# Kernel optimization log

Hardware: AMD Instinct MI355X
Metric: run time of the kernel (lower is better)

The kernel has to match this reference:

```python
import jax, jax.numpy as jnp
import numpy as np

N_NODES = 50000
N_EDGES = 800000
F_DIM = 128
H_DIM = 128


def setup_inputs() -> dict:
    key = jax.random.key(0)
    ks = jax.random.split(key, 14)
    sx = 1.0 / np.sqrt(F_DIM)
    sh = 1.0 / np.sqrt(H_DIM)
    return {
        'x': jax.random.normal(ks[0], (N_NODES, F_DIM), jnp.float32),
        'edge_index': jax.random.randint(ks[1], (2, N_EDGES), 0, N_NODES),
        'edge_weight': jnp.zeros((N_EDGES,), jnp.int32),  # relation ids, all 0 (num_relations=1)
        'h': jax.random.normal(ks[2], (N_NODES, H_DIM), jnp.float32),
        'c': jax.random.normal(ks[3], (N_NODES, H_DIM), jnp.float32),
        # stacked gate params, gate order: i, f, c, o
        'Wx': jax.random.normal(ks[4], (4, F_DIM, H_DIM), jnp.float32) * sx,
        'Wx_root': jax.random.normal(ks[5], (4, F_DIM, H_DIM), jnp.float32) * sx,
        'bx': jax.random.normal(ks[6], (4, H_DIM), jnp.float32) * 0.01,
        'Wh': jax.random.normal(ks[7], (4, H_DIM, H_DIM), jnp.float32) * sh,
        'Wh_root': jax.random.normal(ks[8], (4, H_DIM, H_DIM), jnp.float32) * sh,
        'bh': jax.random.normal(ks[9], (4, H_DIM), jnp.float32) * 0.01,
        'fc_w': jax.random.normal(ks[10], (1, H_DIM), jnp.float32) * sh,
        'fc_b': jax.random.normal(ks[11], (1,), jnp.float32) * 0.01,
    }


def _mean_agg(v, src, dst, n_nodes):
    # scatter-mean of gathered source features onto destination nodes
    s = jax.ops.segment_sum(v[src], dst, num_segments=n_nodes)          # [N, d]
    cnt = jax.ops.segment_sum(jnp.ones(src.shape, v.dtype), dst, num_segments=n_nodes)
    return s / jnp.maximum(cnt, 1.0)[:, None]


def reference(x, edge_index, edge_weight, h, c, Wx, Wx_root, bx, Wh, Wh_root, bh, fc_w, fc_b):
    src, dst = edge_index[0], edge_index[1]
    # single-relation RGCNConv: mean-agg then matmul; aggregation shared across the 4 gates
    agg_x = _mean_agg(x, src, dst, N_NODES)   # [N, F]
    agg_h = _mean_agg(h, src, dst, N_NODES)   # [N, H]
    g = (jnp.einsum('nf,gfh->gnh', agg_x, Wx)
         + jnp.einsum('nf,gfh->gnh', x, Wx_root) + bx[:, None, :]
         + jnp.einsum('nk,gkh->gnh', agg_h, Wh)
         + jnp.einsum('nk,gkh->gnh', h, Wh_root) + bh[:, None, :])  # [4, N, H]
    i_g = jax.nn.sigmoid(g[0])
    f_g = jax.nn.sigmoid(g[1])
    t_g = jnp.tanh(g[2])
    o_g = jax.nn.sigmoid(g[3])
    c_new = f_g * c + i_g * t_g
    h_new = o_g * jnp.tanh(c_new)
    y = jax.nn.relu(h_new) @ fc_w.T + fc_b    # [N, 1]
    return (y, h_new, c_new)
```

## Files before the change

kernel.cpp:

```cpp
#include <hip/hip_runtime.h>
#include <hip/hip_bf16.h>

#define N_NODES 50000
#define N_EDGES 800000
#define FD 128
#define HD 128
#define KTOT 512
#define NTOT 512
#define NRT 391
#define RT_PER_XCD 49
#define SCAN_BLK 1024
#define NSCAN ((N_NODES + SCAN_BLK - 1) / SCAN_BLK)

typedef __attribute__((ext_vector_type(8))) short short8v;
typedef __attribute__((ext_vector_type(8))) __bf16 bf16x8;
typedef __attribute__((ext_vector_type(4))) float f32x4;
typedef __attribute__((ext_vector_type(4))) int i32x4;

__device__ __forceinline__ short f2bf(float f) {
  unsigned u = __builtin_bit_cast(unsigned, f);
  unsigned r = (u + 0x7FFFu + ((u >> 16) & 1u)) >> 16;
  return (short)(r & 0xFFFFu);
}
__device__ __forceinline__ float bf2f(short s) {
  return __builtin_bit_cast(float, ((unsigned)(unsigned short)s) << 16);
}
__device__ __forceinline__ float sigm(float x) {
  return __builtin_amdgcn_rcpf(1.f + __builtin_amdgcn_exp2f(-1.44269504f * x));
}
__device__ __forceinline__ float tanh_(float x) {
  return 1.f - 2.f * __builtin_amdgcn_rcpf(1.f + __builtin_amdgcn_exp2f(2.88539009f * x));
}

__device__ __forceinline__ int swz_col(int c, int r7) {
  return (c & ~63) | (((((c >> 3) & 7) ^ r7)) << 3) | (c & 7);
}

__device__ __forceinline__ void gload_lds16(const void* g, void* l) {
  __builtin_amdgcn_global_load_lds((const __attribute__((address_space(1))) unsigned int*)g,
                                   (__attribute__((address_space(3))) unsigned int*)l, 16, 0, 0);
}

__global__ void k_pre(const float* __restrict__ Wx, const float* __restrict__ Wxr,
                      const float* __restrict__ Wh, const float* __restrict__ Whr,
                      const float* __restrict__ x, const float* __restrict__ h,
                      short* __restrict__ BpackT, short* __restrict__ Apack) {
  int gid = blockIdx.x * 256 + threadIdx.x;
  if (gid < NTOT * KTOT) {
    int col = gid >> 9;
    int k = gid & 511;
    int hb = col >> 7, rem = col & 127;
    int wn = rem >> 6, g = (rem >> 4) & 3, hlow = rem & 15;
    int hid = hb * 32 + wn * 16 + hlow;
    int sel = k >> 7, f = k & 127;
    const float* W = (sel == 0) ? Wx : (sel == 1) ? Wxr : (sel == 2) ? Wh : Whr;
    BpackT[col * KTOT + swz_col(k, col & 7)] = f2bf(W[(g * 128 + f) * 128 + hid]);
  }
  if (gid < N_NODES * 32) {
    int half = gid >= N_NODES * 16;
    int g2 = gid - half * N_NODES * 16;
    int node = g2 >> 4, s = g2 & 15;
    const float* src = (half ? h : x) + (size_t)node * 128 + s * 8;
    f32x4 v0 = *(const f32x4*)(src);
    f32x4 v1 = *(const f32x4*)(src + 4);
    short8v o;
#pragma unroll
    for (int q = 0; q < 4; ++q) { o[q] = f2bf(v0[q]); o[q + 4] = f2bf(v1[q]); }
    int blockbase = 128 + half * 256 + (s >> 3) * 64;
    int slot = (s & 7) ^ (node & 7);
    *(short8v*)(Apack + (size_t)node * KTOT + blockbase + slot * 8) = o;
  }
}

__global__ void k_count(const int* __restrict__ ei, int* __restrict__ cnt,
                        int* __restrict__ rank) {
  int e = blockIdx.x * 256 + threadIdx.x;
  if (e < N_EDGES) rank[e] = atomicAdd(&cnt[ei[N_EDGES + e]], 1);
}

__global__ void k_scanA(const int* __restrict__ cnt, int* __restrict__ bsum) {
  int blk = blockIdx.x, t = threadIdx.x;
  int base = blk * SCAN_BLK + t * 4;
  int s = 0;
  if (base + 3 < N_NODES) {
    i32x4 v = *(const i32x4*)(cnt + base);
    s = v.x + v.y + v.z + v.w;
  }
#pragma unroll
  for (int d = 1; d < 64; d <<= 1) s += __shfl_xor(s, d);
  __shared__ int ws[4];
  if ((t & 63) == 0) ws[t >> 6] = s;
  __syncthreads();
  if (t == 0) bsum[blk] = ws[0] + ws[1] + ws[2] + ws[3];
}

__global__ void k_scanC(const int* __restrict__ cnt, const int* __restrict__ bsum,
                        int* __restrict__ off) {
  __shared__ int sboff[NSCAN];
  int blk = blockIdx.x, t = threadIdx.x;
  if (t < 64) {
    int v = (t < NSCAN) ? bsum[t] : 0;
#pragma unroll
    for (int d = 1; d < 64; d <<= 1) {
      int u = __shfl_up(v, d);
      if (t >= d) v += u;
    }
    if (t < NSCAN) sboff[t] = v;
  }
  __syncthreads();
  int base = blk * SCAN_BLK + t * 4;
  int c0 = 0, c1 = 0, c2 = 0, c3 = 0;
  bool ok = base + 3 < N_NODES;
  if (ok) {
    i32x4 v = *(const i32x4*)(cnt + base);
    c0 = v.x; c1 = v.y; c2 = v.z; c3 = v.w;
  }
  int s = c0 + c1 + c2 + c3;
  int v = s;
#pragma unroll
  for (int d = 1; d < 64; d <<= 1) {
    int u = __shfl_up(v, d);
    if ((t & 63) >= d) v += u;
  }
  __shared__ int wsum[4];
  if ((t & 63) == 63) wsum[t >> 6] = v;
  __syncthreads();
  int wbase = 0;
  for (int w = 0; w < (t >> 6); ++w) wbase += wsum[w];
  int excl = (blk ? sboff[blk - 1] : 0) + wbase + v - s;
  if (ok) {
    i32x4 o = {excl, excl + c0, excl + c0 + c1, excl + c0 + c1 + c2};
    *(i32x4*)(off + base) = o;
  }
  if (blk == 0 && t == 0) off[N_NODES] = N_EDGES;
}

__global__ void k_fill(const int* __restrict__ ei, const int* __restrict__ off,
                       const int* __restrict__ rank, int* __restrict__ elist) {
  int e = blockIdx.x * 256 + threadIdx.x;
  if (e < N_EDGES) {
    int d = ei[N_EDGES + e];
    elist[off[d] + rank[e]] = ei[e];
  }
}

__global__ __launch_bounds__(256) void k_agg_pack(const int* __restrict__ off,
                                                  const int* __restrict__ elist,
                                                  short* __restrict__ Apack) {
  int tid = threadIdx.x;
  int node = blockIdx.x * 4 + (tid >> 6);
  int lane = tid & 63;
  int grp = lane >> 4, l4 = lane & 15;
  int is_h = grp & 1, epair = grp >> 1;
  int b = off[node], e = off[node + 1];
  const int cb = is_h * 256 + 128 + (l4 >> 3) * 64;
  const int sl = l4 & 7;
  float acc[8] = {};
  int j = b;
  for (; j + 8 <= e; j += 8) {
    int s0 = elist[j + epair];
    int s1 = elist[j + 2 + epair];
    int s2 = elist[j + 4 + epair];
    int s3 = elist[j + 6 + epair];
    short8v v0 = *(const short8v*)(Apack + (size_t)s0 * KTOT + cb + ((sl ^ (s0 & 7)) << 3));
    short8v v1 = *(const short8v*)(Apack + (size_t)s1 * KTOT + cb + ((sl ^ (s1 & 7)) << 3));
    short8v v2 = *(const short8v*)(Apack + (size_t)s2 * KTOT + cb + ((sl ^ (s2 & 7)) << 3));
    short8v v3 = *(const short8v*)(Apack + (size_t)s3 * KTOT + cb + ((sl ^ (s3 & 7)) << 3));
#pragma unroll
    for (int q = 0; q < 8; ++q) acc[q] += bf2f(v0[q]);
#pragma unroll
    for (int q = 0; q < 8; ++q) acc[q] += bf2f(v1[q]);
#pragma unroll
    for (int q = 0; q < 8; ++q) acc[q] += bf2f(v2[q]);
#pragma unroll
    for (int q = 0; q < 8; ++q) acc[q] += bf2f(v3[q]);
  }
  for (; j + 2 <= e; j += 2) {
    int s0 = elist[j + epair];
    short8v v0 = *(const short8v*)(Apack + (size_t)s0 * KTOT + cb + ((sl ^ (s0 & 7)) << 3));
#pragma unroll
    for (int q = 0; q < 8; ++q) acc[q] += bf2f(v0[q]);
  }
  if (j < e && epair == 0) {
    int s0 = elist[j];
    short8v v0 = *(const short8v*)(Apack + (size_t)s0 * KTOT + cb + ((sl ^ (s0 & 7)) << 3));
#pragma unroll
    for (int q = 0; q < 8; ++q) acc[q] += bf2f(v0[q]);
  }
#pragma unroll
  for (int q = 0; q < 8; ++q) acc[q] += __shfl_xor(acc[q], 32);
  if (grp < 2) {
    float inv = 1.f / (float)max(e - b, 1);
    int cagg = is_h * 256 + (l4 >> 3) * 64 + ((sl ^ (node & 7)) << 3);
    short8v o;
#pragma unroll
    for (int q = 0; q < 8; ++q) o[q] = f2bf(acc[q] * inv);
    *(short8v*)(Apack + (size_t)node * KTOT + cagg) = o;
  }
}

__global__ __launch_bounds__(512, 4) void k_gemm(
    const short* __restrict__ Apack, const short* __restrict__ BpackT,
    const float* __restrict__ c_in, const float* __restrict__ bx, const float* __restrict__ bh,
    const float* __restrict__ fcw,
    float* __restrict__ hnew, float* __restrict__ cnew, float* __restrict__ ypart) {
  __shared__ short As[2][128 * 64];
  __shared__ short Bs[2][128 * 64];
  const int bid = blockIdx.x;
  const int xcd = bid & 7, q = bid >> 3;
  const int rt = xcd * RT_PER_XCD + (q >> 2);
  const int hb = q & 3;
  if (rt >= NRT) return;
  const int tid = threadIdx.x;
  const int wave = tid >> 6, lane = tid & 63;
  const int l15 = lane & 15, lhi = lane >> 4;
  const int wm = wave & 3, wn = wave >> 2;
  const int row0 = rt * 128;

  const short* Abase = Apack + (size_t)row0 * KTOT;
  const short* Bbase = BpackT + (size_t)hb * 128 * KTOT;
  const int stg_r = tid >> 3;
  const int stg_s = tid & 7;
  const int ldst = (tid & ~63) * 8;

  auto stage = [&](int buf, int k0) {
#pragma unroll
    for (int it = 0; it < 2; ++it) {
      int r = stg_r + it * 64;
      gload_lds16(Abase + (size_t)r * KTOT + k0 + stg_s * 8, &As[buf][ldst + it * 4096]);
      gload_lds16(Bbase + (size_t)r * KTOT + k0 + stg_s * 8, &Bs[buf][ldst + it * 4096]);
    }
  };

  const int rbase = row0 + wm * 32 + lhi * 4;
  const int hid = hb * 32 + wn * 16 + l15;
  float pbi = bx[hid] + bh[hid];
  float pbf = bx[128 + hid] + bh[128 + hid];
  float pbt = bx[256 + hid] + bh[256 + hid];
  float pbo = bx[384 + hid] + bh[384 + hid];
  float pfw = fcw[hid];
  float cpre[2][4];
#pragma unroll
  for (int m = 0; m < 2; ++m)
#pragma unroll
    for (int j = 0; j < 4; ++j) {
      int r = rbase + m * 16 + j;
      cpre[m][j] = (r < N_NODES) ? c_in[(size_t)r * HD + hid] : 0.f;
    }

  f32x4 acc[2][4] = {};

  stage(0, 0);
  __syncthreads();
  int cur = 0;
#pragma unroll
  for (int k0 = 0; k0 < KTOT; k0 += 64) {
    if (k0 + 64 < KTOT) stage(cur ^ 1, k0 + 64);
#pragma unroll
    for (int kk = 0; kk < 2; ++kk) {
      short8v a[2], bfr[4];
      const int sl = ((kk << 2) | lhi) ^ (l15 & 7);
#pragma unroll
      for (int m = 0; m < 2; ++m)
        a[m] = *(const short8v*)(&As[cur][(wm * 32 + m * 16 + l15) * 64 + sl * 8]);
#pragma unroll
      for (int n = 0; n < 4; ++n)
        bfr[n] = *(const short8v*)(&Bs[cur][(wn * 64 + n * 16 + l15) * 64 + sl * 8]);
#pragma unroll
      for (int m = 0; m < 2; ++m)
#pragma unroll
        for (int n = 0; n < 4; ++n)
          acc[m][n] = __builtin_amdgcn_mfma_f32_16x16x32_bf16(
              __builtin_bit_cast(bf16x8, a[m]), __builtin_bit_cast(bf16x8, bfr[n]),
              acc[m][n], 0, 0, 0);
    }
    __syncthreads();
    cur ^= 1;
  }

  float yp[2][4];
#pragma unroll
  for (int m = 0; m < 2; ++m) {
#pragma unroll
    for (int j = 0; j < 4; ++j) {
      int r = rbase + m * 16 + j;
      bool ok = r < N_NODES;
      float ig = sigm(acc[m][0][j] + pbi);
      float fg = sigm(acc[m][1][j] + pbf);
      float tg = tanh_(acc[m][2][j] + pbt);
      float og = sigm(acc[m][3][j] + pbo);
      float cn = fg * cpre[m][j] + ig * tg;
      float hn = og * tanh_(cn);
      if (ok) {
        cnew[(size_t)r * HD + hid] = cn;
        hnew[(size_t)r * HD + hid] = hn;
      }
      yp[m][j] = fmaxf(hn, 0.f) * pfw;
    }
  }
#pragma unroll
  for (int m = 0; m < 2; ++m)
#pragma unroll
    for (int j = 0; j < 4; ++j) {
      float v = yp[m][j];
      v += __shfl_xor(v, 1);
      v += __shfl_xor(v, 2);
      v += __shfl_xor(v, 4);
      v += __shfl_xor(v, 8);
      yp[m][j] = v;
    }
  float* yred = (float*)&As[0][0];
  if (wn == 1 && l15 == 0) {
#pragma unroll
    for (int m = 0; m < 2; ++m)
#pragma unroll
      for (int j = 0; j < 4; ++j)
        yred[wm * 32 + m * 16 + lhi * 4 + j] = yp[m][j];
  }
  __syncthreads();
  if (wn == 0 && l15 == 0) {
#pragma unroll
    for (int m = 0; m < 2; ++m)
#pragma unroll
      for (int j = 0; j < 4; ++j) {
        int r = rbase + m * 16 + j;
        if (r < N_NODES)
          ypart[hb * N_NODES + r] = yp[m][j] + yred[wm * 32 + m * 16 + lhi * 4 + j];
      }
  }
}

__global__ void k_yfinal(const float* __restrict__ ypart, const float* __restrict__ fcb,
                         float* __restrict__ y) {
  int i = blockIdx.x * 256 + threadIdx.x;
  if (i < N_NODES)
    y[i] = fcb[0] + ypart[i] + ypart[N_NODES + i] + ypart[2 * N_NODES + i] + ypart[3 * N_NODES + i];
}

extern "C" void kernel_launch(void* const* d_in, const int* in_sizes, int n_in,
                              void* d_out, int out_size, void* d_ws, size_t ws_size,
                              hipStream_t stream) {
  const float* x   = (const float*)d_in[0];
  const int*   ei  = (const int*)d_in[1];
  const float* h   = (const float*)d_in[3];
  const float* c   = (const float*)d_in[4];
  const float* Wx  = (const float*)d_in[5];
  const float* Wxr = (const float*)d_in[6];
  const float* bx  = (const float*)d_in[7];
  const float* Wh  = (const float*)d_in[8];
  const float* Whr = (const float*)d_in[9];
  const float* bh  = (const float*)d_in[10];
  const float* fcw = (const float*)d_in[11];
  const float* fcb = (const float*)d_in[12];

  float* y    = (float*)d_out;
  float* hnew = y + N_NODES;
  float* cnew = hnew + (size_t)N_NODES * HD;

  char* w = (char*)d_ws;
  auto carve = [&](size_t bytes) {
    char* p = w;
    w += (bytes + 255) & ~(size_t)255;
    return p;
  };
  int* cnt      = (int*)carve((size_t)N_NODES * 4);
  int* off      = (int*)carve((size_t)(N_NODES + 1) * 4);
  int* pos      = (int*)carve((size_t)N_NODES * 4);
  int* elist    = (int*)carve((size_t)N_EDGES * 4);
  short* Apack  = (short*)carve((size_t)N_NODES * KTOT * 2);
  short* BpackT = (short*)carve((size_t)NTOT * KTOT * 2);
  float* ypart  = (float*)carve((size_t)4 * N_NODES * 4);
  int* bsum     = (int*)ypart;
  int* rank     = (int*)Apack;
  (void)pos;

  hipMemsetAsync(cnt, 0, (size_t)N_NODES * 4, stream);
  k_count<<<(N_EDGES + 255) / 256, 256, 0, stream>>>(ei, cnt, rank);
  k_scanA<<<NSCAN, 256, 0, stream>>>(cnt, bsum);
  k_scanC<<<NSCAN, 256, 0, stream>>>(cnt, bsum, off);
  k_fill<<<(N_EDGES + 255) / 256, 256, 0, stream>>>(ei, off, rank, elist);
  k_pre<<<(N_NODES * 32 + 255) / 256, 256, 0, stream>>>(Wx, Wxr, Wh, Whr, x, h, BpackT, Apack);
  k_agg_pack<<<(N_NODES + 3) / 4, 256, 0, stream>>>(off, elist, Apack);
  dim3 gg(8 * RT_PER_XCD * 4);
  k_gemm<<<gg, 512, 0, stream>>>(Apack, BpackT, c, bx, bh, fcw, hnew, cnew, ypart);
  k_yfinal<<<(N_NODES + 255) / 256, 256, 0, stream>>>(ypart, fcb, y);
}
```

Baseline: 179.0 us.

## Fuse edge counting into pre-pack kernel and split gather into two source-range phases

The edge-count atomics move into k_pre, removing one launch. Ranks are now stored in the unused aggregate slots (first 128 columns) of Apack rows so they survive the bf16 packing of x/h. The aggregation kernel now makes two passes over each node's edge list, gathering only sources from one half of the node range per pass, to improve L2 locality of the random gathers. The cost is reading the index list twice plus extra branch and predication work.

```diff
diff --git a/kernel.cpp b/kernel.cpp
--- a/kernel.cpp
+++ b/kernel.cpp
@@ -44,8 +44,15 @@
 __global__ void k_pre(const float* __restrict__ Wx, const float* __restrict__ Wxr,
                       const float* __restrict__ Wh, const float* __restrict__ Whr,
                       const float* __restrict__ x, const float* __restrict__ h,
-                      short* __restrict__ BpackT, short* __restrict__ Apack) {
+                      const int* __restrict__ ei,
+                      short* __restrict__ BpackT, short* __restrict__ Apack,
+                      int* __restrict__ cnt) {
   int gid = blockIdx.x * 256 + threadIdx.x;
+  if (gid < N_EDGES) {
+    int d = ei[N_EDGES + gid];
+    int r = atomicAdd(&cnt[d], 1);
+    ((int*)(Apack + (size_t)(gid >> 6) * KTOT))[gid & 63] = r;
+  }
   if (gid < NTOT * KTOT) {
     int col = gid >> 9;
     int k = gid & 511;
@@ -72,12 +79,6 @@
   }
 }
 
-__global__ void k_count(const int* __restrict__ ei, int* __restrict__ cnt,
-                        int* __restrict__ rank) {
-  int e = blockIdx.x * 256 + threadIdx.x;
-  if (e < N_EDGES) rank[e] = atomicAdd(&cnt[ei[N_EDGES + e]], 1);
-}
-
 __global__ void k_scanA(const int* __restrict__ cnt, int* __restrict__ bsum) {
   int blk = blockIdx.x, t = threadIdx.x;
   int base = blk * SCAN_BLK + t * 4;
@@ -136,11 +137,12 @@
 }
 
 __global__ void k_fill(const int* __restrict__ ei, const int* __restrict__ off,
-                       const int* __restrict__ rank, int* __restrict__ elist) {
+                       const short* __restrict__ Apack, int* __restrict__ elist) {
   int e = blockIdx.x * 256 + threadIdx.x;
   if (e < N_EDGES) {
     int d = ei[N_EDGES + e];
-    elist[off[d] + rank[e]] = ei[e];
+    int rk = ((const int*)(Apack + (size_t)(e >> 6) * KTOT))[e & 63];
+    elist[off[d] + rk] = ei[e];
   }
 }
 
@@ -156,36 +158,49 @@
   const int cb = is_h * 256 + 128 + (l4 >> 3) * 64;
   const int sl = l4 & 7;
   float acc[8] = {};
-  int j = b;
-  for (; j + 8 <= e; j += 8) {
-    int s0 = elist[j + epair];
-    int s1 = elist[j + 2 + epair];
-    int s2 = elist[j + 4 + epair];
-    int s3 = elist[j + 6 + epair];
-    short8v v0 = *(const short8v*)(Apack + (size_t)s0 * KTOT + cb + ((sl ^ (s0 & 7)) << 3));
-    short8v v1 = *(const short8v*)(Apack + (size_t)s1 * KTOT + cb + ((sl ^ (s1 & 7)) << 3));
-    short8v v2 = *(const short8v*)(Apack + (size_t)s2 * KTOT + cb + ((sl ^ (s2 & 7)) << 3));
-    short8v v3 = *(const short8v*)(Apack + (size_t)s3 * KTOT + cb + ((sl ^ (s3 & 7)) << 3));
-#pragma unroll
-    for (int q = 0; q < 8; ++q) acc[q] += bf2f(v0[q]);
-#pragma unroll
-    for (int q = 0; q < 8; ++q) acc[q] += bf2f(v1[q]);
-#pragma unroll
-    for (int q = 0; q < 8; ++q) acc[q] += bf2f(v2[q]);
-#pragma unroll
-    for (int q = 0; q < 8; ++q) acc[q] += bf2f(v3[q]);
-  }
-  for (; j + 2 <= e; j += 2) {
-    int s0 = elist[j + epair];
-    short8v v0 = *(const short8v*)(Apack + (size_t)s0 * KTOT + cb + ((sl ^ (s0 & 7)) << 3));
-#pragma unroll
-    for (int q = 0; q < 8; ++q) acc[q] += bf2f(v0[q]);
-  }
-  if (j < e && epair == 0) {
-    int s0 = elist[j];
-    short8v v0 = *(const short8v*)(Apack + (size_t)s0 * KTOT + cb + ((sl ^ (s0 & 7)) << 3));
-#pragma unroll
-    for (int q = 0; q < 8; ++q) acc[q] += bf2f(v0[q]);
+#pragma unroll
+  for (int ph = 0; ph < 2; ++ph) {
+    const int lo = ph * (N_NODES / 2);
+    int j = b;
+    for (; j + 8 <= e; j += 8) {
+      int s0 = elist[j + epair];
+      int s1 = elist[j + 2 + epair];
+      int s2 = elist[j + 4 + epair];
+      int s3 = elist[j + 6 + epair];
+      bool c0 = (unsigned)(s0 - lo) < (unsigned)(N_NODES / 2);
+      bool c1 = (unsigned)(s1 - lo) < (unsigned)(N_NODES / 2);
+      bool c2 = (unsigned)(s2 - lo) < (unsigned)(N_NODES / 2);
+      bool c3 = (unsigned)(s3 - lo) < (unsigned)(N_NODES / 2);
+      short8v v0 = (short8v)0, v1 = (short8v)0, v2 = (short8v)0, v3 = (short8v)0;
+      if (c0) v0 = *(const short8v*)(Apack + (size_t)s0 * KTOT + cb + ((sl ^ (s0 & 7)) << 3));
+      if (c1) v1 = *(const short8v*)(Apack + (size_t)s1 * KTOT + cb + ((sl ^ (s1 & 7)) << 3));
+      if (c2) v2 = *(const short8v*)(Apack + (size_t)s2 * KTOT + cb + ((sl ^ (s2 & 7)) << 3));
+      if (c3) v3 = *(const short8v*)(Apack + (size_t)s3 * KTOT + cb + ((sl ^ (s3 & 7)) << 3));
+#pragma unroll
+      for (int q = 0; q < 8; ++q) acc[q] += bf2f(v0[q]);
+#pragma unroll
+      for (int q = 0; q < 8; ++q) acc[q] += bf2f(v1[q]);
+#pragma unroll
+      for (int q = 0; q < 8; ++q) acc[q] += bf2f(v2[q]);
+#pragma unroll
+      for (int q = 0; q < 8; ++q) acc[q] += bf2f(v3[q]);
+    }
+    for (; j + 2 <= e; j += 2) {
+      int s0 = elist[j + epair];
+      if ((unsigned)(s0 - lo) < (unsigned)(N_NODES / 2)) {
+        short8v v0 = *(const short8v*)(Apack + (size_t)s0 * KTOT + cb + ((sl ^ (s0 & 7)) << 3));
+#pragma unroll
+        for (int q = 0; q < 8; ++q) acc[q] += bf2f(v0[q]);
+      }
+    }
+    if (j < e && epair == 0) {
+      int s0 = elist[j];
+      if ((unsigned)(s0 - lo) < (unsigned)(N_NODES / 2)) {
+        short8v v0 = *(const short8v*)(Apack + (size_t)s0 * KTOT + cb + ((sl ^ (s0 & 7)) << 3));
+#pragma unroll
+        for (int q = 0; q < 8; ++q) acc[q] += bf2f(v0[q]);
+      }
+    }
   }
 #pragma unroll
   for (int q = 0; q < 8; ++q) acc[q] += __shfl_xor(acc[q], 32);
@@ -371,15 +386,14 @@
   short* BpackT = (short*)carve((size_t)NTOT * KTOT * 2);
   float* ypart  = (float*)carve((size_t)4 * N_NODES * 4);
   int* bsum     = (int*)ypart;
-  int* rank     = (int*)Apack;
   (void)pos;
 
   hipMemsetAsync(cnt, 0, (size_t)N_NODES * 4, stream);
-  k_count<<<(N_EDGES + 255) / 256, 256, 0, stream>>>(ei, cnt, rank);
+  k_pre<<<(N_NODES * 32 + 255) / 256, 256, 0, stream>>>(Wx, Wxr, Wh, Whr, x, h, ei,
+                                                        BpackT, Apack, cnt);
   k_scanA<<<NSCAN, 256, 0, stream>>>(cnt, bsum);
   k_scanC<<<NSCAN, 256, 0, stream>>>(cnt, bsum, off);
-  k_fill<<<(N_EDGES + 255) / 256, 256, 0, stream>>>(ei, off, rank, elist);
-  k_pre<<<(N_NODES * 32 + 255) / 256, 256, 0, stream>>>(Wx, Wxr, Wh, Whr, x, h, BpackT, Apack);
+  k_fill<<<(N_EDGES + 255) / 256, 256, 0, stream>>>(ei, off, Apack, elist);
   k_agg_pack<<<(N_NODES + 3) / 4, 256, 0, stream>>>(off, elist, Apack);
   dim3 gg(8 * RT_PER_XCD * 4);
   k_gemm<<<gg, 512, 0, stream>>>(Apack, BpackT, c, bx, bh, fcw, hnew, cnew, ypart);
```

Measured after the change: 185.5 us. 1.04x slower.
